# Performance work log

Measured on AMD Instinct MI355X. Metric: run time of the kernel, lower is better.

## Reference

```python
import jax, jax.numpy as jnp
import numpy as np

NUM_USER = 200000
NUM_ITEM = 100000
DIM = 64
NUM_LAYER = 2  # hardcoded in LightGCN.__init__ (lgn_single(..., num_layer=2))
AVG_DEG = 16
N = NUM_USER + NUM_ITEM
E = N * AVG_DEG
BATCH = 16384


def setup_inputs() -> dict:
    key = jax.random.key(0)
    k = jax.random.split(key, 8)
    emb_user = jax.random.normal(k[0], (NUM_USER, DIM), jnp.float32) * 0.05
    emb_item = jax.random.normal(k[1], (NUM_ITEM, DIM), jnp.float32) * 0.05
    # COO sparse normalized adjacency: out[row] += vals * x[col]
    graph_row = jax.random.randint(k[2], (E,), 0, N, dtype=jnp.int32)
    graph_col = jax.random.randint(k[3], (E,), 0, N, dtype=jnp.int32)
    graph_vals = jax.random.uniform(k[4], (E,), jnp.float32) / AVG_DEG
    user_nodes = jax.random.randint(k[5], (BATCH,), 0, NUM_USER, dtype=jnp.int32)
    pos_item_nodes = jax.random.randint(k[6], (BATCH,), 0, NUM_ITEM, dtype=jnp.int32) + NUM_USER
    neg_item_nodes = jax.random.randint(k[7], (BATCH,), 0, NUM_ITEM, dtype=jnp.int32) + NUM_USER
    return {
        "emb_user": emb_user,
        "emb_item": emb_item,
        "graph_vals": graph_vals,
        "graph_row": graph_row,
        "graph_col": graph_col,
        "user_nodes": user_nodes,
        "pos_item_nodes": pos_item_nodes,
        "neg_item_nodes": neg_item_nodes,
    }


def _spmm(vals, row, col, x):
    # torch.sparse.mm(graph, x) with graph in COO form
    return jax.ops.segment_sum(vals[:, None] * x[col], row, num_segments=N)


def reference(emb_user, emb_item, graph_vals, graph_row, graph_col,
              user_nodes, pos_item_nodes, neg_item_nodes):
    # LGN_single.forward: concat, propagate, mean over layer stack
    all_emb = jnp.concatenate([emb_user, emb_item], axis=0)  # [N, D]
    acc = all_emb
    e = all_emb
    for _ in range(NUM_LAYER):
        e = _spmm(graph_vals, graph_row, graph_col, e)
        acc = acc + e
    light_out = acc / (NUM_LAYER + 1)  # mean of stacked embeddings
    # LightGCN.forward: gather + elementwise dot scores
    u = light_out[user_nodes]          # [B, D]
    p = light_out[pos_item_nodes]      # [B, D]
    n = light_out[neg_item_nodes]      # [B, D]
    pos_scores = jnp.sum(u * p, axis=1)
    neg_scores = jnp.sum(u * n, axis=1)
    return jnp.stack([pos_scores, neg_scores])  # [2, B]
```

## Files before the change

### kernel.cpp

```cpp
#include <hip/hip_runtime.h>

#define DIM 64
#define CHUNK 4096
#define MAXNB 2048
#define PADSLOP 1792
#define P2CAP 7680

__device__ __forceinline__ unsigned short f2bf(float f) {
    unsigned int u = __float_as_uint(f);
    return (unsigned short)((u + 0x7FFFu + ((u >> 16) & 1u)) >> 16);
}
__device__ __forceinline__ float4 bf2f4(uint2 g) {
    float4 x;
    x.x = __uint_as_float(g.x << 16);
    x.y = __uint_as_float(g.x & 0xffff0000u);
    x.z = __uint_as_float(g.y << 16);
    x.w = __uint_as_float(g.y & 0xffff0000u);
    return x;
}

__device__ __forceinline__ int blockScan256(int v, int* sh) {
    int t = threadIdx.x;
    sh[t] = v;
    __syncthreads();
    for (int off = 1; off < 256; off <<= 1) {
        int x = (t >= off) ? sh[t - off] : 0;
        __syncthreads();
        sh[t] += x;
        __syncthreads();
    }
    return sh[t];
}


__global__ void conv2_k(const float* __restrict__ u, const float* __restrict__ it,
                        int nu, int ntot, unsigned short* __restrict__ o) {
    int i = blockIdx.x * blockDim.x + threadIdx.x;
    int stride = gridDim.x * blockDim.x;
    int n8 = ntot >> 3;
    for (int t = i; t < n8; t += stride) {
        int e = t * 8;
        const float* src = (e < nu) ? (u + e) : (it + (e - nu));
        float4 x = *(const float4*)src;
        float4 y = *(const float4*)(src + 4);
        uint4 v;
        v.x = (unsigned)f2bf(x.x) | ((unsigned)f2bf(x.y) << 16);
        v.y = (unsigned)f2bf(x.z) | ((unsigned)f2bf(x.w) << 16);
        v.z = (unsigned)f2bf(y.x) | ((unsigned)f2bf(y.y) << 16);
        v.w = (unsigned)f2bf(y.z) | ((unsigned)f2bf(y.w) << 16);
        ((uint4*)o)[t] = v;
    }
}


__global__ void p1a_hist(const int* __restrict__ row, int E, int NB,
                         int* __restrict__ counts) {
    __shared__ int h[MAXNB];
    for (int b = threadIdx.x; b < NB; b += 256) h[b] = 0;
    __syncthreads();
    int base = blockIdx.x * CHUNK;
    int end = min(base + CHUNK, E);
    int vend = base + ((end - base) & ~3);
    for (int i = base + threadIdx.x * 4; i < vend; i += 1024) {
        int4 r = *(const int4*)(row + i);
        atomicAdd(&h[r.x >> 8], 1);
        atomicAdd(&h[r.y >> 8], 1);
        atomicAdd(&h[r.z >> 8], 1);
        atomicAdd(&h[r.w >> 8], 1);
    }
    for (int i = vend + threadIdx.x; i < end; i += 256) atomicAdd(&h[row[i] >> 8], 1);
    __syncthreads();
    int blk = blockIdx.x;
    for (int b = threadIdx.x; b < NB; b += 256) counts[(size_t)blk * NB + b] = h[b];
}

__global__ void p1b_scan(int* __restrict__ counts, int NBLK, int NB,
                         int* __restrict__ bucketTotal) {
    int b = blockIdx.x, t = threadIdx.x;
    __shared__ int sh[256];
    int v[8];
    int run = 0;
#pragma unroll
    for (int i = 0; i < 8; i++) {
        int idx = t * 8 + i;
        int c = (idx < NBLK) ? counts[(size_t)idx * NB + b] : 0;
        v[i] = run;
        run += c;
    }
    int inc = blockScan256(run, sh);
    int excl = inc - run;
#pragma unroll
    for (int i = 0; i < 8; i++) {
        int idx = t * 8 + i;
        if (idx < NBLK) counts[(size_t)idx * NB + b] = v[i] + excl;
    }
    if (t == 255) bucketTotal[b] = sh[255];
}

__global__ void p_scan_tot(const int* __restrict__ bucketTotal, int NB,
                           int* __restrict__ bucketStart) {
    int t = threadIdx.x;
    __shared__ int sh[256];
    int v[8];
    int run = 0;
#pragma unroll
    for (int i = 0; i < 8; i++) {
        int idx = t * 8 + i;
        int c = (idx < NB) ? bucketTotal[idx] : 0;
        v[i] = run;
        run += c;
    }
    int inc = blockScan256(run, sh);
    int excl = inc - run;
#pragma unroll
    for (int i = 0; i < 8; i++) {
        int idx = t * 8 + i;
        if (idx < NB) bucketStart[idx] = v[i] + excl;
    }
    if (t == 255) bucketStart[NB] = sh[255];
}

__global__ void p1c_scatter(const int* __restrict__ row, const int* __restrict__ col,
                            const float* __restrict__ vals, int E, int NB,
                            const int* __restrict__ counts, const int* __restrict__ bucketStart,
                            int2* __restrict__ bdata) {
    __shared__ int cur[MAXNB];
    int blk = blockIdx.x;
    for (int b = threadIdx.x; b < NB; b += 256)
        cur[b] = bucketStart[b] + counts[(size_t)blk * NB + b];
    __syncthreads();
    int base = blk * CHUNK;
    int end = min(base + CHUNK, E);
    int vend = base + ((end - base) & ~3);
    for (int i = base + threadIdx.x * 4; i < vend; i += 1024) {
        int4 r = *(const int4*)(row + i);
        int4 c = *(const int4*)(col + i);
        float4 v = *(const float4*)(vals + i);
        int p0 = atomicAdd(&cur[r.x >> 8], 1);
        int p1 = atomicAdd(&cur[r.y >> 8], 1);
        int p2 = atomicAdd(&cur[r.z >> 8], 1);
        int p3 = atomicAdd(&cur[r.w >> 8], 1);
        bdata[p0] = make_int2(((r.x & 255) << 20) | c.x, __float_as_int(v.x));
        bdata[p1] = make_int2(((r.y & 255) << 20) | c.y, __float_as_int(v.y));
        bdata[p2] = make_int2(((r.z & 255) << 20) | c.z, __float_as_int(v.z));
        bdata[p3] = make_int2(((r.w & 255) << 20) | c.w, __float_as_int(v.w));
    }
    for (int i = vend + threadIdx.x; i < end; i += 256) {
        int r = row[i];
        int p = atomicAdd(&cur[r >> 8], 1);
        bdata[p] = make_int2(((r & 255) << 20) | col[i], __float_as_int(vals[i]));
    }
}

__global__ void p2_group(const int2* __restrict__ bdata, const int* __restrict__ bucketStart,
                         int NB, int N,
                         int* __restrict__ rowStart, int* __restrict__ rowLen,
                         int2* __restrict__ pairs) {
    __shared__ int hist[256];
    __shared__ int sh[256];
    __shared__ int cur[256];
    __shared__ int2 stage[P2CAP];
    int b = blockIdx.x, t = threadIdx.x;
    int s0 = bucketStart[b], s1 = bucketStart[b + 1];
    int pbase = s0 + b * PADSLOP;
    hist[t] = 0;
    __syncthreads();
    for (int i = s0 + t; i < s1; i += 256)
        atomicAdd(&hist[(bdata[i].x >> 20) & 255], 1);
    __syncthreads();
    int h = hist[t];
    int hp = (h + 7) & ~7;
    int inc = blockScan256(hp, sh);
    int excl = inc - hp;
    int ptot = sh[255];
    int r = b * 256 + t;
    if (r < N) {
        rowStart[r] = pbase + excl;
        rowLen[r] = hp;
    }
    cur[t] = excl;
    __syncthreads();
    if (ptot <= P2CAP) {
        for (int i = t; i < ptot; i += 256) stage[i] = make_int2(0, 0);
        __syncthreads();
        for (int i = s0 + t; i < s1; i += 256) {
            int2 e = bdata[i];
            int rl = (e.x >> 20) & 255;
            int pos = atomicAdd(&cur[rl], 1);
            stage[pos] = make_int2((e.x & 0xFFFFF) << 7, e.y);
        }
        __syncthreads();
        for (int i = t; i < ptot; i += 256) pairs[pbase + i] = stage[i];
    } else {
        for (int i = t; i < ptot; i += 256) pairs[pbase + i] = make_int2(0, 0);
        __syncthreads();
        for (int i = s0 + t; i < s1; i += 256) {
            int2 e = bdata[i];
            int rl = (e.x >> 20) & 255;
            int pos = atomicAdd(&cur[rl], 1);
            pairs[pbase + pos] = make_int2((e.x & 0xFFFFF) << 7, e.y);
        }
    }
}


__global__ void spmm1_k(const unsigned short* __restrict__ emb16,
                        const int* __restrict__ rowStart, const int* __restrict__ rowLen,
                        const int2* __restrict__ pairs,
                        int n_total, unsigned short* __restrict__ e1) {
    int wave = (blockIdx.x * blockDim.x + threadIdx.x) >> 6;
    int lane = threadIdx.x & 63;
    if (wave >= n_total) return;
    int eg = lane >> 4, dp = lane & 15;
    unsigned off0 = dp * 8u;
    const char* base = (const char*)emb16;
    int len = rowLen[wave];
    const int2* pp = pairs + rowStart[wave];
    float4 a0 = {0.f, 0.f, 0.f, 0.f}, a1 = {0.f, 0.f, 0.f, 0.f};
    for (int k = 0; k < len; k += 8) {
        int2 p0 = pp[k + eg];
        int2 p1 = pp[k + 4 + eg];
        uint2 g0 = *(const uint2*)(base + ((unsigned)p0.x + off0));
        uint2 g1 = *(const uint2*)(base + ((unsigned)p1.x + off0));
        float v0 = __int_as_float(p0.y);
        float v1 = __int_as_float(p1.y);
        float4 x0 = bf2f4(g0);
        float4 x1 = bf2f4(g1);
        a0.x += v0 * x0.x; a0.y += v0 * x0.y; a0.z += v0 * x0.z; a0.w += v0 * x0.w;
        a1.x += v1 * x1.x; a1.y += v1 * x1.y; a1.z += v1 * x1.z; a1.w += v1 * x1.w;
    }
    float4 s;
    s.x = a0.x + a1.x; s.y = a0.y + a1.y; s.z = a0.z + a1.z; s.w = a0.w + a1.w;
    s.x += __shfl_xor(s.x, 16); s.y += __shfl_xor(s.y, 16);
    s.z += __shfl_xor(s.z, 16); s.w += __shfl_xor(s.w, 16);
    s.x += __shfl_xor(s.x, 32); s.y += __shfl_xor(s.y, 32);
    s.z += __shfl_xor(s.z, 32); s.w += __shfl_xor(s.w, 32);
    if (eg == 0) {
        uint2 o;
        o.x = (unsigned)f2bf(s.x) | ((unsigned)f2bf(s.y) << 16);
        o.y = (unsigned)f2bf(s.z) | ((unsigned)f2bf(s.w) << 16);
        *(uint2*)(e1 + (size_t)wave * DIM + dp * 4) = o;
    }
}


__global__ void final_k(const float* __restrict__ emb_user, const float* __restrict__ emb_item,
                        int n_user, const unsigned short* __restrict__ e1,
                        const int* __restrict__ rowStart, const int* __restrict__ rowLen,
                        const int2* __restrict__ pairs,
                        const int* __restrict__ u_nodes, const int* __restrict__ p_nodes,
                        const int* __restrict__ n_nodes, int B, float* __restrict__ out) {
    int wave = (blockIdx.x * blockDim.x + threadIdx.x) >> 6;
    int lane = threadIdx.x & 63;
    if (wave >= B) return;
    int eg = lane >> 4, dp = lane & 15;
    unsigned off0 = dp * 8u;
    const char* base = (const char*)e1;
    int nid[3] = {u_nodes[wave], p_nodes[wave], n_nodes[wave]};
    float4 l[3];
#pragma unroll
    for (int j = 0; j < 3; j++) {
        int r = nid[j];
        const float* base0 = (r < n_user) ? (emb_user + (size_t)r * DIM)
                                          : (emb_item + (size_t)(r - n_user) * DIM);
        float4 acc = *(const float4*)(base0 + dp * 4);
        float4 t1 = bf2f4(*(const uint2*)(e1 + (size_t)r * DIM + dp * 4));
        acc.x += t1.x; acc.y += t1.y; acc.z += t1.z; acc.w += t1.w;
        int len = rowLen[r];
        const int2* pp = pairs + rowStart[r];
        float4 a0 = {0.f, 0.f, 0.f, 0.f}, a1 = {0.f, 0.f, 0.f, 0.f};
        for (int k = 0; k < len; k += 8) {
            int2 p0 = pp[k + eg];
            int2 p1 = pp[k + 4 + eg];
            uint2 g0 = *(const uint2*)(base + ((unsigned)p0.x + off0));
            uint2 g1 = *(const uint2*)(base + ((unsigned)p1.x + off0));
            float v0 = __int_as_float(p0.y);
            float v1 = __int_as_float(p1.y);
            float4 x0 = bf2f4(g0);
            float4 x1 = bf2f4(g1);
            a0.x += v0 * x0.x; a0.y += v0 * x0.y; a0.z += v0 * x0.z; a0.w += v0 * x0.w;
            a1.x += v1 * x1.x; a1.y += v1 * x1.y; a1.z += v1 * x1.z; a1.w += v1 * x1.w;
        }
        float4 s;
        s.x = a0.x + a1.x; s.y = a0.y + a1.y; s.z = a0.z + a1.z; s.w = a0.w + a1.w;
        s.x += __shfl_xor(s.x, 16); s.y += __shfl_xor(s.y, 16);
        s.z += __shfl_xor(s.z, 16); s.w += __shfl_xor(s.w, 16);
        s.x += __shfl_xor(s.x, 32); s.y += __shfl_xor(s.y, 32);
        s.z += __shfl_xor(s.z, 32); s.w += __shfl_xor(s.w, 32);
        l[j].x = (acc.x + s.x) * (1.0f / 3.0f);
        l[j].y = (acc.y + s.y) * (1.0f / 3.0f);
        l[j].z = (acc.z + s.z) * (1.0f / 3.0f);
        l[j].w = (acc.w + s.w) * (1.0f / 3.0f);
    }
    float ps = l[0].x * l[1].x + l[0].y * l[1].y + l[0].z * l[1].z + l[0].w * l[1].w;
    float ns = l[0].x * l[2].x + l[0].y * l[2].y + l[0].z * l[2].z + l[0].w * l[2].w;
    ps += __shfl_xor(ps, 1); ns += __shfl_xor(ns, 1);
    ps += __shfl_xor(ps, 2); ns += __shfl_xor(ns, 2);
    ps += __shfl_xor(ps, 4); ns += __shfl_xor(ns, 4);
    ps += __shfl_xor(ps, 8); ns += __shfl_xor(ns, 8);
    if (lane == 0) {
        out[wave] = ps;
        out[B + wave] = ns;
    }
}

extern "C" void kernel_launch(void* const* d_in, const int* in_sizes, int n_in,
                              void* d_out, int out_size, void* d_ws, size_t ws_size,
                              hipStream_t stream) {
    const float* emb_user = (const float*)d_in[0];
    const float* emb_item = (const float*)d_in[1];
    const float* gvals    = (const float*)d_in[2];
    const int*   grow     = (const int*)d_in[3];
    const int*   gcol     = (const int*)d_in[4];
    const int*   unodes   = (const int*)d_in[5];
    const int*   pnodes   = (const int*)d_in[6];
    const int*   nnodes   = (const int*)d_in[7];
    float* out = (float*)d_out;

    int n_user = in_sizes[0] / DIM;
    int n_item = in_sizes[1] / DIM;
    int N = n_user + n_item;
    int E = in_sizes[2];
    int B = in_sizes[5];
    int NB = (N + 255) >> 8;
    int NBLK = (E + CHUNK - 1) / CHUNK;

    char* ws = (char*)d_ws;
    size_t off = 0;
    auto alloc = [&](size_t bytes) -> void* {
        void* p = ws + off;
        off = (off + bytes + 255) & ~(size_t)255;
        return p;
    };
    int*  rowStart    = (int*)alloc((size_t)N * 4);
    int*  rowLen      = (int*)alloc((size_t)N * 4);
    int*  bucketTotal = (int*)alloc((size_t)MAXNB * 4);
    int*  bucketStart = (int*)alloc((size_t)(MAXNB + 1) * 4);
    int2* pairs       = (int2*)alloc(((size_t)E + (size_t)NB * PADSLOP) * 8);
    char* regionB = (char*)alloc((size_t)E * 8 > (size_t)N * DIM * 2 ? (size_t)E * 8
                                                                     : (size_t)N * DIM * 2);
    int2*           bdata = (int2*)regionB;
    unsigned short* emb16 = (unsigned short*)regionB;
    size_t countsBytes = (size_t)NBLK * NB * 4;
    size_t e1Bytes = (size_t)N * DIM * 2;
    char* regionA = (char*)alloc(countsBytes > e1Bytes ? countsBytes : e1Bytes);
    int*            counts = (int*)regionA;
    unsigned short* e1     = (unsigned short*)regionA;
    (void)ws_size; (void)n_in; (void)out_size;

    p1a_hist<<<NBLK, 256, 0, stream>>>(grow, E, NB, counts);
    p1b_scan<<<NB, 256, 0, stream>>>(counts, NBLK, NB, bucketTotal);
    p_scan_tot<<<1, 256, 0, stream>>>(bucketTotal, NB, bucketStart);
    p1c_scatter<<<NBLK, 256, 0, stream>>>(grow, gcol, gvals, E, NB, counts, bucketStart, bdata);
    p2_group<<<NB, 256, 0, stream>>>(bdata, bucketStart, NB, N, rowStart, rowLen, pairs);

    conv2_k<<<2048, 256, 0, stream>>>(emb_user, emb_item, n_user * DIM, N * DIM, emb16);

    spmm1_k<<<(N + 3) / 4, 256, 0, stream>>>(emb16, rowStart, rowLen, pairs, N, e1);
    final_k<<<(B + 3) / 4, 256, 0, stream>>>(emb_user, emb_item, n_user, e1,
                                             rowStart, rowLen, pairs,
                                             unodes, pnodes, nnodes, B, out);
}
```

Before: 313.9 us.

## Widen row buckets to 1024 rows, pad rows to 16 edges, unroll SpMM gathers

Buckets for the CSR build now hold 1024 rows instead of 256, cutting the bucket count and the per-block histogram traffic. The shared-memory staging path in the grouping kernel is dropped, and rows are padded to multiples of 16 when the workspace allows, falling back to 8 otherwise. Both SpMM loops process 16 edges per iteration with four accumulators, giving more independent gathers in flight. The cost is extra zero-padding work and bandwidth, plus more atomic contention in the grouping kernel, which now writes straight to global memory.

```diff
diff --git a/kernel.cpp b/kernel.cpp
--- a/kernel.cpp
+++ b/kernel.cpp
@@ -2,9 +2,10 @@
 
 #define DIM 64
 #define CHUNK 4096
-#define MAXNB 2048
-#define PADSLOP 1792
-#define P2CAP 7680
+#define MAXNB 512
+#define MAXNBLK 2048
+#define BSHIFT 10
+#define RPB 1024
 
 __device__ __forceinline__ unsigned short f2bf(float f) {
     unsigned int u = __float_as_uint(f);
@@ -63,12 +64,12 @@
     int vend = base + ((end - base) & ~3);
     for (int i = base + threadIdx.x * 4; i < vend; i += 1024) {
         int4 r = *(const int4*)(row + i);
-        atomicAdd(&h[r.x >> 8], 1);
-        atomicAdd(&h[r.y >> 8], 1);
-        atomicAdd(&h[r.z >> 8], 1);
-        atomicAdd(&h[r.w >> 8], 1);
-    }
-    for (int i = vend + threadIdx.x; i < end; i += 256) atomicAdd(&h[row[i] >> 8], 1);
+        atomicAdd(&h[r.x >> BSHIFT], 1);
+        atomicAdd(&h[r.y >> BSHIFT], 1);
+        atomicAdd(&h[r.z >> BSHIFT], 1);
+        atomicAdd(&h[r.w >> BSHIFT], 1);
+    }
+    for (int i = vend + threadIdx.x; i < end; i += 256) atomicAdd(&h[row[i] >> BSHIFT], 1);
     __syncthreads();
     int blk = blockIdx.x;
     for (int b = threadIdx.x; b < NB; b += 256) counts[(size_t)blk * NB + b] = h[b];
@@ -136,70 +137,68 @@
         int4 r = *(const int4*)(row + i);
         int4 c = *(const int4*)(col + i);
         float4 v = *(const float4*)(vals + i);
-        int p0 = atomicAdd(&cur[r.x >> 8], 1);
-        int p1 = atomicAdd(&cur[r.y >> 8], 1);
-        int p2 = atomicAdd(&cur[r.z >> 8], 1);
-        int p3 = atomicAdd(&cur[r.w >> 8], 1);
-        bdata[p0] = make_int2(((r.x & 255) << 20) | c.x, __float_as_int(v.x));
-        bdata[p1] = make_int2(((r.y & 255) << 20) | c.y, __float_as_int(v.y));
-        bdata[p2] = make_int2(((r.z & 255) << 20) | c.z, __float_as_int(v.z));
-        bdata[p3] = make_int2(((r.w & 255) << 20) | c.w, __float_as_int(v.w));
+        int p0 = atomicAdd(&cur[r.x >> BSHIFT], 1);
+        int p1 = atomicAdd(&cur[r.y >> BSHIFT], 1);
+        int p2 = atomicAdd(&cur[r.z >> BSHIFT], 1);
+        int p3 = atomicAdd(&cur[r.w >> BSHIFT], 1);
+        bdata[p0] = make_int2(((r.x & (RPB - 1)) << 20) | c.x, __float_as_int(v.x));
+        bdata[p1] = make_int2(((r.y & (RPB - 1)) << 20) | c.y, __float_as_int(v.y));
+        bdata[p2] = make_int2(((r.z & (RPB - 1)) << 20) | c.z, __float_as_int(v.z));
+        bdata[p3] = make_int2(((r.w & (RPB - 1)) << 20) | c.w, __float_as_int(v.w));
     }
     for (int i = vend + threadIdx.x; i < end; i += 256) {
         int r = row[i];
-        int p = atomicAdd(&cur[r >> 8], 1);
-        bdata[p] = make_int2(((r & 255) << 20) | col[i], __float_as_int(vals[i]));
+        int p = atomicAdd(&cur[r >> BSHIFT], 1);
+        bdata[p] = make_int2(((r & (RPB - 1)) << 20) | col[i], __float_as_int(vals[i]));
     }
 }
 
 __global__ void p2_group(const int2* __restrict__ bdata, const int* __restrict__ bucketStart,
-                         int NB, int N,
+                         int NB, int N, int padMask, int padSlop,
                          int* __restrict__ rowStart, int* __restrict__ rowLen,
                          int2* __restrict__ pairs) {
-    __shared__ int hist[256];
+    __shared__ int hist[RPB];
     __shared__ int sh[256];
-    __shared__ int cur[256];
-    __shared__ int2 stage[P2CAP];
+    __shared__ int cur[RPB];
     int b = blockIdx.x, t = threadIdx.x;
     int s0 = bucketStart[b], s1 = bucketStart[b + 1];
-    int pbase = s0 + b * PADSLOP;
-    hist[t] = 0;
+    int pbase = s0 + b * padSlop;
+    for (int i = t; i < RPB; i += 256) hist[i] = 0;
     __syncthreads();
     for (int i = s0 + t; i < s1; i += 256)
-        atomicAdd(&hist[(bdata[i].x >> 20) & 255], 1);
-    __syncthreads();
-    int h = hist[t];
-    int hp = (h + 7) & ~7;
-    int inc = blockScan256(hp, sh);
-    int excl = inc - hp;
+        atomicAdd(&hist[(bdata[i].x >> 20) & (RPB - 1)], 1);
+    __syncthreads();
+    int v[4];
+    int run = 0;
+#pragma unroll
+    for (int i = 0; i < 4; i++) {
+        int h = hist[t * 4 + i];
+        int hp = (h + padMask) & ~padMask;
+        v[i] = run;
+        run += hp;
+    }
+    int inc = blockScan256(run, sh);
+    int excl = inc - run;
     int ptot = sh[255];
-    int r = b * 256 + t;
-    if (r < N) {
-        rowStart[r] = pbase + excl;
-        rowLen[r] = hp;
-    }
-    cur[t] = excl;
-    __syncthreads();
-    if (ptot <= P2CAP) {
-        for (int i = t; i < ptot; i += 256) stage[i] = make_int2(0, 0);
-        __syncthreads();
-        for (int i = s0 + t; i < s1; i += 256) {
-            int2 e = bdata[i];
-            int rl = (e.x >> 20) & 255;
-            int pos = atomicAdd(&cur[rl], 1);
-            stage[pos] = make_int2((e.x & 0xFFFFF) << 7, e.y);
+#pragma unroll
+    for (int i = 0; i < 4; i++) {
+        int r = (b << BSHIFT) + t * 4 + i;
+        int st = excl + v[i];
+        if (r < N) {
+            int h = hist[t * 4 + i];
+            rowStart[r] = pbase + st;
+            rowLen[r] = (h + padMask) & ~padMask;
         }
-        __syncthreads();
-        for (int i = t; i < ptot; i += 256) pairs[pbase + i] = stage[i];
-    } else {
-        for (int i = t; i < ptot; i += 256) pairs[pbase + i] = make_int2(0, 0);
-        __syncthreads();
-        for (int i = s0 + t; i < s1; i += 256) {
-            int2 e = bdata[i];
-            int rl = (e.x >> 20) & 255;
-            int pos = atomicAdd(&cur[rl], 1);
-            pairs[pbase + pos] = make_int2((e.x & 0xFFFFF) << 7, e.y);
-        }
+        cur[t * 4 + i] = st;
+    }
+    __syncthreads();
+    for (int i = t; i < ptot; i += 256) pairs[pbase + i] = make_int2(0, 0);
+    __syncthreads();
+    for (int i = s0 + t; i < s1; i += 256) {
+        int2 e = bdata[i];
+        int rl = (e.x >> 20) & (RPB - 1);
+        int pos = atomicAdd(&cur[rl], 1);
+        pairs[pbase + pos] = make_int2((e.x & 0xFFFFF) << 7, e.y);
     }
 }
 
@@ -217,20 +216,40 @@
     int len = rowLen[wave];
     const int2* pp = pairs + rowStart[wave];
     float4 a0 = {0.f, 0.f, 0.f, 0.f}, a1 = {0.f, 0.f, 0.f, 0.f};
-    for (int k = 0; k < len; k += 8) {
+    float4 a2 = {0.f, 0.f, 0.f, 0.f}, a3 = {0.f, 0.f, 0.f, 0.f};
+    int k = 0;
+    for (; k + 16 <= len; k += 16) {
+        int2 p0 = pp[k + eg];
+        int2 p1 = pp[k + 4 + eg];
+        int2 p2 = pp[k + 8 + eg];
+        int2 p3 = pp[k + 12 + eg];
+        uint2 g0 = *(const uint2*)(base + ((unsigned)p0.x + off0));
+        uint2 g1 = *(const uint2*)(base + ((unsigned)p1.x + off0));
+        uint2 g2 = *(const uint2*)(base + ((unsigned)p2.x + off0));
+        uint2 g3 = *(const uint2*)(base + ((unsigned)p3.x + off0));
+        float v0 = __int_as_float(p0.y), v1 = __int_as_float(p1.y);
+        float v2 = __int_as_float(p2.y), v3 = __int_as_float(p3.y);
+        float4 x0 = bf2f4(g0), x1 = bf2f4(g1), x2 = bf2f4(g2), x3 = bf2f4(g3);
+        a0.x += v0 * x0.x; a0.y += v0 * x0.y; a0.z += v0 * x0.z; a0.w += v0 * x0.w;
+        a1.x += v1 * x1.x; a1.y += v1 * x1.y; a1.z += v1 * x1.z; a1.w += v1 * x1.w;
+        a2.x += v2 * x2.x; a2.y += v2 * x2.y; a2.z += v2 * x2.z; a2.w += v2 * x2.w;
+        a3.x += v3 * x3.x; a3.y += v3 * x3.y; a3.z += v3 * x3.z; a3.w += v3 * x3.w;
+    }
+    for (; k < len; k += 8) {
         int2 p0 = pp[k + eg];
         int2 p1 = pp[k + 4 + eg];
         uint2 g0 = *(const uint2*)(base + ((unsigned)p0.x + off0));
         uint2 g1 = *(const uint2*)(base + ((unsigned)p1.x + off0));
-        float v0 = __int_as_float(p0.y);
-        float v1 = __int_as_float(p1.y);
-        float4 x0 = bf2f4(g0);
-        float4 x1 = bf2f4(g1);
+        float v0 = __int_as_float(p0.y), v1 = __int_as_float(p1.y);
+        float4 x0 = bf2f4(g0), x1 = bf2f4(g1);
         a0.x += v0 * x0.x; a0.y += v0 * x0.y; a0.z += v0 * x0.z; a0.w += v0 * x0.w;
         a1.x += v1 * x1.x; a1.y += v1 * x1.y; a1.z += v1 * x1.z; a1.w += v1 * x1.w;
     }
     float4 s;
-    s.x = a0.x + a1.x; s.y = a0.y + a1.y; s.z = a0.z + a1.z; s.w = a0.w + a1.w;
+    s.x = (a0.x + a1.x) + (a2.x + a3.x);
+    s.y = (a0.y + a1.y) + (a2.y + a3.y);
+    s.z = (a0.z + a1.z) + (a2.z + a3.z);
+    s.w = (a0.w + a1.w) + (a2.w + a3.w);
     s.x += __shfl_xor(s.x, 16); s.y += __shfl_xor(s.y, 16);
     s.z += __shfl_xor(s.z, 16); s.w += __shfl_xor(s.w, 16);
     s.x += __shfl_xor(s.x, 32); s.y += __shfl_xor(s.y, 32);
@@ -269,20 +288,40 @@
         int len = rowLen[r];
         const int2* pp = pairs + rowStart[r];
         float4 a0 = {0.f, 0.f, 0.f, 0.f}, a1 = {0.f, 0.f, 0.f, 0.f};
-        for (int k = 0; k < len; k += 8) {
+        float4 a2 = {0.f, 0.f, 0.f, 0.f}, a3 = {0.f, 0.f, 0.f, 0.f};
+        int k = 0;
+        for (; k + 16 <= len; k += 16) {
+            int2 p0 = pp[k + eg];
+            int2 p1 = pp[k + 4 + eg];
+            int2 p2 = pp[k + 8 + eg];
+            int2 p3 = pp[k + 12 + eg];
+            uint2 g0 = *(const uint2*)(base + ((unsigned)p0.x + off0));
+            uint2 g1 = *(const uint2*)(base + ((unsigned)p1.x + off0));
+            uint2 g2 = *(const uint2*)(base + ((unsigned)p2.x + off0));
+            uint2 g3 = *(const uint2*)(base + ((unsigned)p3.x + off0));
+            float v0 = __int_as_float(p0.y), v1 = __int_as_float(p1.y);
+            float v2 = __int_as_float(p2.y), v3 = __int_as_float(p3.y);
+            float4 x0 = bf2f4(g0), x1 = bf2f4(g1), x2 = bf2f4(g2), x3 = bf2f4(g3);
+            a0.x += v0 * x0.x; a0.y += v0 * x0.y; a0.z += v0 * x0.z; a0.w += v0 * x0.w;
+            a1.x += v1 * x1.x; a1.y += v1 * x1.y; a1.z += v1 * x1.z; a1.w += v1 * x1.w;
+            a2.x += v2 * x2.x; a2.y += v2 * x2.y; a2.z += v2 * x2.z; a2.w += v2 * x2.w;
+            a3.x += v3 * x3.x; a3.y += v3 * x3.y; a3.z += v3 * x3.z; a3.w += v3 * x3.w;
+        }
+        for (; k < len; k += 8) {
             int2 p0 = pp[k + eg];
             int2 p1 = pp[k + 4 + eg];
             uint2 g0 = *(const uint2*)(base + ((unsigned)p0.x + off0));
             uint2 g1 = *(const uint2*)(base + ((unsigned)p1.x + off0));
-            float v0 = __int_as_float(p0.y);
-            float v1 = __int_as_float(p1.y);
-            float4 x0 = bf2f4(g0);
-            float4 x1 = bf2f4(g1);
+            float v0 = __int_as_float(p0.y), v1 = __int_as_float(p1.y);
+            float4 x0 = bf2f4(g0), x1 = bf2f4(g1);
             a0.x += v0 * x0.x; a0.y += v0 * x0.y; a0.z += v0 * x0.z; a0.w += v0 * x0.w;
             a1.x += v1 * x1.x; a1.y += v1 * x1.y; a1.z += v1 * x1.z; a1.w += v1 * x1.w;
         }
         float4 s;
-        s.x = a0.x + a1.x; s.y = a0.y + a1.y; s.z = a0.z + a1.z; s.w = a0.w + a1.w;
+        s.x = (a0.x + a1.x) + (a2.x + a3.x);
+        s.y = (a0.y + a1.y) + (a2.y + a3.y);
+        s.z = (a0.z + a1.z) + (a2.z + a3.z);
+        s.w = (a0.w + a1.w) + (a2.w + a3.w);
         s.x += __shfl_xor(s.x, 16); s.y += __shfl_xor(s.y, 16);
         s.z += __shfl_xor(s.z, 16); s.w += __shfl_xor(s.w, 16);
         s.x += __shfl_xor(s.x, 32); s.y += __shfl_xor(s.y, 32);
@@ -322,8 +361,24 @@
     int N = n_user + n_item;
     int E = in_sizes[2];
     int B = in_sizes[5];
-    int NB = (N + 255) >> 8;
+    int NB = (N + RPB - 1) >> BSHIFT;
     int NBLK = (E + CHUNK - 1) / CHUNK;
+
+    auto align256 = [](size_t x) { return (x + 255) & ~(size_t)255; };
+    size_t embBytes = (size_t)N * DIM * 2;
+    size_t countsBytes = (size_t)NBLK * NB * 4;
+    size_t regionBBytes = (size_t)E * 8 > embBytes ? (size_t)E * 8 : embBytes;
+    size_t regionABytes = countsBytes > embBytes ? countsBytes : embBytes;
+    size_t fixedBytes = align256((size_t)N * 4) + align256((size_t)N * 4) +
+                        align256((size_t)MAXNB * 4) + align256((size_t)(MAXNB + 1) * 4) +
+                        align256(regionBBytes) + align256(regionABytes);
+    int padMask = 15;
+    size_t pairsBytes = ((size_t)E + (size_t)NB * RPB * padMask) * 8;
+    if (fixedBytes + align256(pairsBytes) > ws_size) {
+        padMask = 7;
+        pairsBytes = ((size_t)E + (size_t)NB * RPB * padMask) * 8;
+    }
+    int padSlop = RPB * padMask;
 
     char* ws = (char*)d_ws;
     size_t off = 0;
@@ -336,23 +391,21 @@
     int*  rowLen      = (int*)alloc((size_t)N * 4);
     int*  bucketTotal = (int*)alloc((size_t)MAXNB * 4);
     int*  bucketStart = (int*)alloc((size_t)(MAXNB + 1) * 4);
-    int2* pairs       = (int2*)alloc(((size_t)E + (size_t)NB * PADSLOP) * 8);
-    char* regionB = (char*)alloc((size_t)E * 8 > (size_t)N * DIM * 2 ? (size_t)E * 8
-                                                                     : (size_t)N * DIM * 2);
+    int2* pairs       = (int2*)alloc(pairsBytes);
+    char* regionB = (char*)alloc(regionBBytes);
     int2*           bdata = (int2*)regionB;
     unsigned short* emb16 = (unsigned short*)regionB;
-    size_t countsBytes = (size_t)NBLK * NB * 4;
-    size_t e1Bytes = (size_t)N * DIM * 2;
-    char* regionA = (char*)alloc(countsBytes > e1Bytes ? countsBytes : e1Bytes);
+    char* regionA = (char*)alloc(regionABytes);
     int*            counts = (int*)regionA;
     unsigned short* e1     = (unsigned short*)regionA;
-    (void)ws_size; (void)n_in; (void)out_size;
+    (void)n_in; (void)out_size;
 
     p1a_hist<<<NBLK, 256, 0, stream>>>(grow, E, NB, counts);
     p1b_scan<<<NB, 256, 0, stream>>>(counts, NBLK, NB, bucketTotal);
     p_scan_tot<<<1, 256, 0, stream>>>(bucketTotal, NB, bucketStart);
     p1c_scatter<<<NBLK, 256, 0, stream>>>(grow, gcol, gvals, E, NB, counts, bucketStart, bdata);
-    p2_group<<<NB, 256, 0, stream>>>(bdata, bucketStart, NB, N, rowStart, rowLen, pairs);
+    p2_group<<<NB, 256, 0, stream>>>(bdata, bucketStart, NB, N, padMask, padSlop,
+                                     rowStart, rowLen, pairs);
 
     conv2_k<<<2048, 256, 0, stream>>>(emb_user, emb_item, n_user * DIM, N * DIM, emb16);
 
```

New measurement: 328.8 us. +4.8%, slower.
